# Performance work log

Measured on AMD Instinct MI355X. Metric: run time of the kernel, lower is better.

## Reference

```python
import jax, jax.numpy as jnp
import numpy as np

D_MODEL = 512
D_STATE = 64
N_LAYERS = 6
L_SEQ = 784
BATCH = 64


def _layernorm(x, g, b, eps=1e-5):
    mu = x.mean(-1, keepdims=True)
    var = ((x - mu) ** 2).mean(-1, keepdims=True)
    return (x - mu) * jax.lax.rsqrt(var + eps) * g + b


def _s4d_kernel(log_dt, log_A_real, A_imag, C_re, C_im, L):
    # log_dt: (H,), others: (H, N). Returns real conv kernel (H, L).
    dt = jnp.exp(log_dt)[:, None]                      # (H,1)
    A = -jnp.exp(log_A_real) + 1j * A_imag             # (H,N) complex
    C = C_re + 1j * C_im                               # (H,N)
    dtA = A * dt                                       # (H,N)
    Cd = C * (jnp.exp(dtA) - 1.0) / A                  # ZOH-discretized C
    # Vandermonde: V[h,n,l] = exp(dtA[h,n] * l)
    V = jnp.exp(dtA[:, :, None] * jnp.arange(L, dtype=jnp.float32))  # (H,N,L)
    K = 2.0 * jnp.einsum('hn,hnl->hl', Cd, V).real     # (H,L)
    return K


def _s4_fftconv(u, K, D):
    # u: (B,L,H), K: (H,L), D: (H,)
    L = u.shape[1]
    uf = jnp.fft.rfft(u, 2 * L, axis=1)                # (B, L+1, H)
    kf = jnp.fft.rfft(K.T, 2 * L, axis=0)              # (L+1, H)
    y = jnp.fft.irfft(uf * kf[None], 2 * L, axis=1)[:, :L]
    return y + u * D


def setup_inputs() -> dict:
    key = jax.random.key(0)
    ks = jax.random.split(key, 12)
    H, N, NL = D_MODEL, D_STATE, N_LAYERS
    x = jax.random.normal(ks[0], (BATCH, L_SEQ, 1), dtype=jnp.float32)
    enc_w = jax.random.normal(ks[1], (1, H), dtype=jnp.float32) * 0.5
    enc_b = jnp.zeros((H,), dtype=jnp.float32)
    # S4D-Lin style init, stacked over layers
    log_dt = jnp.tile(
        jax.random.uniform(ks[2], (H,), minval=np.log(0.001), maxval=np.log(0.1)),
        (NL, 1))                                        # (NL,H)
    log_A_real = jnp.full((NL, H, N), jnp.log(0.5), dtype=jnp.float32)
    A_imag = jnp.tile(np.pi * jnp.arange(N, dtype=jnp.float32), (NL, H, 1))
    C_re = jax.random.normal(ks[3], (NL, H, N), dtype=jnp.float32) * (0.5 ** 0.5)
    C_im = jax.random.normal(ks[4], (NL, H, N), dtype=jnp.float32) * (0.5 ** 0.5)
    D = jax.random.normal(ks[5], (NL, H), dtype=jnp.float32)
    ln_g = jnp.ones((NL, H), dtype=jnp.float32)
    ln_b = jnp.zeros((NL, H), dtype=jnp.float32)
    fn_g = jnp.ones((H,), dtype=jnp.float32)
    fn_b = jnp.zeros((H,), dtype=jnp.float32)
    dec_w = jax.random.normal(ks[6], (H, 10), dtype=jnp.float32) / jnp.sqrt(H)
    dec_b = jnp.zeros((10,), dtype=jnp.float32)
    return dict(x=x, enc_w=enc_w, enc_b=enc_b, log_dt=log_dt,
                log_A_real=log_A_real, A_imag=A_imag, C_re=C_re, C_im=C_im,
                D=D, ln_g=ln_g, ln_b=ln_b, fn_g=fn_g, fn_b=fn_b,
                dec_w=dec_w, dec_b=dec_b)


def reference(x, enc_w, enc_b, log_dt, log_A_real, A_imag, C_re, C_im, D,
              ln_g, ln_b, fn_g, fn_b, dec_w, dec_b):
    h = x @ enc_w + enc_b                               # (B,L,H)
    L = h.shape[1]
    for i in range(log_dt.shape[0]):                    # fixed n_layers
        K = _s4d_kernel(log_dt[i], log_A_real[i], A_imag[i], C_re[i], C_im[i], L)
        z = _s4_fftconv(h, K, D[i])                     # S4 output (dropout=eval)
        h = _layernorm(h + z, ln_g[i], ln_b[i])         # residual + LN
    h = _layernorm(h, fn_g, fn_b)
    h = h.mean(axis=1)                                  # mean pool over seq
    return h @ dec_w + dec_b                            # (B,10)
```

## Files before the change

kernel.cpp:

```cpp
#include <hip/hip_runtime.h>
#include <hip/hip_bf16.h>

#define HD 512
#define NST 64
#define NLAY 6
#define LSEQ 784
#define BB 64
#define NKA 848
#define TOFF 800
#define LPADROWS 800
#define KSTR 850
#define CHK2 5
#define NCH 5
#define UTS2 9

typedef unsigned short u16;
typedef short s8v __attribute__((ext_vector_type(8)));
typedef float f16v __attribute__((ext_vector_type(16)));
typedef u16  u4h __attribute__((ext_vector_type(4)));
typedef u16  u8h __attribute__((ext_vector_type(8)));

__device__ __forceinline__ unsigned f2b(float f)
{
    unsigned u = __builtin_bit_cast(unsigned, f);
    return (u + 0x7FFFu + ((u >> 16) & 1u)) >> 16;
}
__device__ __forceinline__ float b2f16(u16 v)
{
    unsigned u = ((unsigned)v) << 16;
    return __builtin_bit_cast(float, u);
}

__global__ void precompute_k(const float* __restrict__ log_dt,
                             const float* __restrict__ log_A_real,
                             const float* __restrict__ A_imag,
                             const float* __restrict__ C_re,
                             const float* __restrict__ C_im,
                             float* __restrict__ lamr, float* __restrict__ lami,
                             float* __restrict__ dtr,  float* __restrict__ dti,
                             float* __restrict__ c2r,  float* __restrict__ c2i)
{
    int t = blockIdx.x * 256 + threadIdx.x;
    if (t >= NLAY * HD * NST) return;
    int ih = t >> 6;
    float dt  = expf(log_dt[ih]);
    float are = -expf(log_A_real[t]);
    float aim = A_imag[t];
    float dr = are * dt, di = aim * dt;
    float er = expf(dr);
    float sn, cs; __sincosf(di, &sn, &cs);
    float lr = er * cs, li = er * sn;
    float e1r = lr - 1.0f, e1i = li;
    float den = are * are + aim * aim;
    float qr = (e1r * are + e1i * aim) / den;
    float qi = (e1i * are - e1r * aim) / den;
    float crv = C_re[t], civ = C_im[t];
    lamr[t] = lr; lami[t] = li; dtr[t] = dr; dti[t] = di;
    c2r[t] = 2.0f * (crv * qr - civ * qi);
    c2i[t] = 2.0f * (crv * qi + civ * qr);
}

__global__ void kq_k(const float* __restrict__ lamr, const float* __restrict__ lami,
                     const float* __restrict__ dtr,  const float* __restrict__ dti,
                     const float* __restrict__ c2r,  const float* __restrict__ c2i,
                     u16* __restrict__ KA)
{
    int t = blockIdx.x * 256 + threadIdx.x;
    int dc = t % 49;
    int ih = t / 49;
    int d0 = dc * 16;
    float acc[16];
#pragma unroll
    for (int k = 0; k < 16; k++) acc[k] = 0.f;
    int base = ih * 64;
    for (int n = 0; n < 64; n += 4) {
        float lr[4], li[4], cr[4], ci[4], pr[4], pi[4];
#pragma unroll
        for (int j = 0; j < 4; j++) {
            int q = base + n + j;
            lr[j] = lamr[q]; li[j] = lami[q];
            float dr = dtr[q], di = dti[q];
            cr[j] = c2r[q]; ci[j] = c2i[q];
            float e = __expf(dr * (float)d0);
            float sn, cs; __sincosf(di * (float)d0, &sn, &cs);
            pr[j] = e * cs; pi[j] = e * sn;
        }
#pragma unroll
        for (int k = 0; k < 16; k++) {
#pragma unroll
            for (int j = 0; j < 4; j++) {
                acc[k] = fmaf(cr[j], pr[j], fmaf(-ci[j], pi[j], acc[k]));
                float nr = pr[j] * lr[j] - pi[j] * li[j];
                pi[j] = fmaf(pr[j], li[j], pi[j] * lr[j]);
                pr[j] = nr;
            }
        }
    }
    u16* kap = KA + (size_t)ih * NKA;
#pragma unroll
    for (int k = 0; k < 16; k++)
        kap[TOFF - (d0 + k)] = (u16)f2b(acc[k]);
    if (dc == 0)  for (int z = TOFF + 1; z < NKA; z++) kap[z] = 0;
    if (dc == 48) for (int z = 0; z < TOFF - 783; z++) kap[z] = 0;
}

__global__ void xt_k(const float* __restrict__ x, float* __restrict__ xT)
{
    int t = blockIdx.x * 256 + threadIdx.x;
    int l = t >> 6, b = t & 63;
    xT[t] = x[b * LSEQ + l];
}

__global__ void encoder_k(const float* __restrict__ xT, const float* __restrict__ ew,
                          const float* __restrict__ eb, u16* __restrict__ Vb)
{
    int g = blockIdx.x * 256 + threadIdx.x;
    int bo = g & 7;
    int h  = (g >> 3) & 511;
    int l  = g >> 12;
    uint4* dst = (uint4*)&Vb[((size_t)l * HD + h) * BB + 8 * bo];
    if (l >= LSEQ) { *dst = (uint4){0, 0, 0, 0}; return; }
    const float4* xp = (const float4*)&xT[l * BB + 8 * bo];
    float4 a0 = xp[0], a1 = xp[1];
    float w = ew[h], bb = eb[h];
    unsigned p0 = f2b(fmaf(a0.x, w, bb)) | (f2b(fmaf(a0.y, w, bb)) << 16);
    unsigned p1 = f2b(fmaf(a0.z, w, bb)) | (f2b(fmaf(a0.w, w, bb)) << 16);
    unsigned p2 = f2b(fmaf(a1.x, w, bb)) | (f2b(fmaf(a1.y, w, bb)) << 16);
    unsigned p3 = f2b(fmaf(a1.z, w, bb)) | (f2b(fmaf(a1.w, w, bb)) << 16);
    *dst = (uint4){p0, p1, p2, p3};
}

__global__ __launch_bounds__(128, 4)
void conv_k(const u16* __restrict__ Vb, u16* __restrict__ V2,
            const u16* __restrict__ KA, const float* __restrict__ Dvec)
{
    __shared__ __align__(16) u16 KR[6816];
    __shared__ __align__(16) unsigned UT[2][64 * UTS2];

    const int thr = threadIdx.x;
    const int h   = blockIdx.x & 511;
    const int c   = NCH - 1 - (blockIdx.x >> 9);
    const int w   = thr >> 6;
    const int lane = thr & 63;
    const int n2 = lane & 31;
    const int qp = lane >> 5;
    const int JTN = 10 * c + 10;

    const u16* kap = KA + (size_t)h * NKA;
    {
        int s = thr & 7, ch = thr >> 3;
        int i0 = ch * 53;
        int i1 = (i0 + 53 < NKA) ? (i0 + 53) : NKA;
        u16* kr = KR + KSTR * s + ((8 - s) & 7);
        for (int i = i0; i < i1; i++) kr[i] = kap[i];
    }

    const int jj = thr >> 4;
    const int bq = thr & 15;
    {
        const u16* p = &Vb[((size_t)(2 * jj) * HD + h) * BB + 4 * bq];
        u4h r0 = *(const u4h*)p;
        u4h r1 = *(const u4h*)(p + (size_t)HD * BB);
        unsigned* up = &UT[0][0];
#pragma unroll
        for (int i = 0; i < 4; i++)
            up[(4 * bq + i) * UTS2 + jj] = (unsigned)r0[i] | ((unsigned)r1[i] << 16);
    }
    __syncthreads();

    f16v acc[CHK2];
#pragma unroll
    for (int i = 0; i < CHK2; i++)
#pragma unroll
        for (int r = 0; r < 16; r++) acc[i][r] = 0.f;

    const float dcoef = 1.0f + Dvec[h];

    const int s = lane & 7;
    const u16* krb = KR + KSTR * s + ((8 - s) & 7)
                     + (TOFF - 160 * c) + 8 * qp - n2;
    const unsigned* bb0 = &UT[0][(32 * w + n2) * UTS2 + 4 * qp];
    const unsigned* bb1 = &UT[1][(32 * w + n2) * UTS2 + 4 * qp];

    for (int jt = 0; jt < JTN; ++jt) {
        u4h r0, r1;
        const bool more = (jt + 1) < JTN;
        if (more) {
            int j = 16 * (jt + 1) + 2 * jj;
            const u16* p = &Vb[((size_t)j * HD + h) * BB + 4 * bq];
            r0 = *(const u4h*)p;
            r1 = *(const u4h*)(p + (size_t)HD * BB);
        }
        const unsigned* bb = (jt & 1) ? bb1 : bb0;
        union { unsigned u[4]; s8v v; } bu;
        bu.u[0] = bb[0]; bu.u[1] = bb[1]; bu.u[2] = bb[2]; bu.u[3] = bb[3];

        const u16* ap0 = krb + 16 * jt;
#pragma unroll
        for (int lt = 0; lt < CHK2; ++lt) {
            if (jt > 10 * c + 2 * lt + 1) continue;
            s8v av = *(const s8v*)__builtin_assume_aligned(ap0 - 32 * lt, 16);
            acc[lt] = __builtin_amdgcn_mfma_f32_32x32x16_bf16(av, bu.v, acc[lt], 0, 0, 0);
        }
        if (more) {
            unsigned* up = &UT[(jt & 1) ^ 1][0];
#pragma unroll
            for (int i = 0; i < 4; i++)
                up[(4 * bq + i) * UTS2 + jj] = (unsigned)r0[i] | ((unsigned)r1[i] << 16);
        }
        __syncthreads();
    }

#pragma unroll
    for (int lt = 0; lt < CHK2; ++lt) {
        const int l0 = 32 * (5 * c + lt) + 4 * qp;
#pragma unroll
        for (int r = 0; r < 16; ++r) {
            int l = l0 + (r & 3) + 8 * (r >> 2);
            size_t a = ((size_t)l * HD + h) * BB + 32 * w + n2;
            V2[a] = (u16)f2b(fmaf(dcoef, b2f16(Vb[a]), acc[lt][r]));
        }
    }
}

__global__ __launch_bounds__(512)
void lnT_k(const u16* __restrict__ src, u16* __restrict__ dst,
           const float* __restrict__ gp, const float* __restrict__ bp)
{
    __shared__ float redS[64][65], redQ[64][65];
    __shared__ float mus[64], rss[64];
    __shared__ float gs[512], bs[512];
    const int thr = threadIdx.x;
    const int bo = thr & 7;
    const int hg = thr >> 3;
    const size_t l = blockIdx.x;
    gs[thr] = gp[thr]; bs[thr] = bp[thr];

    const u16* sp = &src[(l * HD + hg * 8) * BB + 8 * bo];
    float v[64];
    float s[8] = {0, 0, 0, 0, 0, 0, 0, 0};
    float q[8] = {0, 0, 0, 0, 0, 0, 0, 0};
#pragma unroll
    for (int k = 0; k < 8; k++) {
        u8h r = *(const u8h*)(sp + (size_t)k * BB);
#pragma unroll
        for (int i = 0; i < 8; i++) {
            float x = b2f16(r[i]);
            v[k * 8 + i] = x;
            s[i] += x;
            q[i] = fmaf(x, x, q[i]);
        }
    }
#pragma unroll
    for (int i = 0; i < 8; i++) { redS[hg][8 * bo + i] = s[i]; redQ[hg][8 * bo + i] = q[i]; }
    __syncthreads();
    if (thr < 64) {
        float ts = 0.f, tq = 0.f;
#pragma unroll
        for (int g = 0; g < 64; g++) { ts += redS[g][thr]; tq += redQ[g][thr]; }
        float mu = ts * (1.0f / HD);
        mus[thr] = mu;
        rss[thr] = rsqrtf(tq * (1.0f / HD) - mu * mu + 1e-5f);
    }
    __syncthreads();
    float mu[8], rs[8];
#pragma unroll
    for (int i = 0; i < 8; i++) { mu[i] = mus[8 * bo + i]; rs[i] = rss[8 * bo + i]; }
    u16* dp = &dst[(l * HD + hg * 8) * BB + 8 * bo];
#pragma unroll
    for (int k = 0; k < 8; k++) {
        float g = gs[hg * 8 + k], bb = bs[hg * 8 + k];
        u8h w;
#pragma unroll
        for (int i = 0; i < 8; i++)
            w[i] = (u16)f2b(fmaf((v[k * 8 + i] - mu[i]) * rs[i], g, bb));
        *(u8h*)(dp + (size_t)k * BB) = w;
    }
}

__global__ __launch_bounds__(512)
void lnT2s_k(const u16* __restrict__ src, u16* __restrict__ dst,
             const float* __restrict__ g5p, const float* __restrict__ b5p,
             const float* __restrict__ gp, const float* __restrict__ bp)
{
    __shared__ float redS[64][65], redQ[64][65];
    __shared__ float mu1s[64], rs1s[64], mu2s[64], rs2s[64];
    __shared__ float gs[512], bs[512];
    const int thr = threadIdx.x;
    const int bo = thr & 7;
    const int hg = thr >> 3;
    const size_t l = blockIdx.x;
    gs[thr] = gp[thr]; bs[thr] = bp[thr];

    const u16* sp = &src[(l * HD + (size_t)hg * 8) * BB + 8 * bo];
    float v[64];
    float s[8] = {0, 0, 0, 0, 0, 0, 0, 0};
    float q[8] = {0, 0, 0, 0, 0, 0, 0, 0};
#pragma unroll
    for (int k = 0; k < 8; k++) {
        u8h r = *(const u8h*)(sp + (size_t)k * BB);
#pragma unroll
        for (int i = 0; i < 8; i++) {
            float x = b2f16(r[i]);
            v[k * 8 + i] = x;
            s[i] += x;
            q[i] = fmaf(x, x, q[i]);
        }
    }
#pragma unroll
    for (int i = 0; i < 8; i++) { redS[hg][8 * bo + i] = s[i]; redQ[hg][8 * bo + i] = q[i]; }
    __syncthreads();
    if (thr < 64) {
        float ts = 0.f, tq = 0.f;
#pragma unroll
        for (int g = 0; g < 64; g++) { ts += redS[g][thr]; tq += redQ[g][thr]; }
        float mu = ts * (1.0f / HD);
        mu1s[thr] = mu;
        rs1s[thr] = rsqrtf(tq * (1.0f / HD) - mu * mu + 1e-5f);
    }
    __syncthreads();
    float mu1[8], rs1[8];
#pragma unroll
    for (int i = 0; i < 8; i++) { mu1[i] = mu1s[8 * bo + i]; rs1[i] = rs1s[8 * bo + i]; }

    float s2[8] = {0, 0, 0, 0, 0, 0, 0, 0};
    float q2[8] = {0, 0, 0, 0, 0, 0, 0, 0};
#pragma unroll
    for (int k = 0; k < 8; k++) {
        float g5 = g5p[hg * 8 + k], b5 = b5p[hg * 8 + k];
#pragma unroll
        for (int i = 0; i < 8; i++) {
            float x = fmaf((v[k * 8 + i] - mu1[i]) * rs1[i], g5, b5);
            v[k * 8 + i] = x;
            s2[i] += x;
            q2[i] = fmaf(x, x, q2[i]);
        }
    }
#pragma unroll
    for (int i = 0; i < 8; i++) { redS[hg][8 * bo + i] = s2[i]; redQ[hg][8 * bo + i] = q2[i]; }
    __syncthreads();
    if (thr < 64) {
        float ts = 0.f, tq = 0.f;
#pragma unroll
        for (int g = 0; g < 64; g++) { ts += redS[g][thr]; tq += redQ[g][thr]; }
        float mu = ts * (1.0f / HD);
        mu2s[thr] = mu;
        rs2s[thr] = rsqrtf(tq * (1.0f / HD) - mu * mu + 1e-5f);
    }
    __syncthreads();
    float mu2[8], rs2[8];
#pragma unroll
    for (int i = 0; i < 8; i++) { mu2[i] = mu2s[8 * bo + i]; rs2[i] = rs2s[8 * bo + i]; }
    u16* dp = &dst[(l * HD + (size_t)hg * 8) * BB + 8 * bo];
#pragma unroll
    for (int k = 0; k < 8; k++) {
        float g = gs[hg * 8 + k], bb = bs[hg * 8 + k];
        u8h wv;
#pragma unroll
        for (int i = 0; i < 8; i++)
            wv[i] = (u16)f2b(fmaf((v[k * 8 + i] - mu2[i]) * rs2[i], g, bb));
        *(u8h*)(dp + (size_t)k * BB) = wv;
    }
}

__global__ __launch_bounds__(256)
void pool2_k(const u16* __restrict__ Vb, float* __restrict__ PO2)
{
    const int cb = blockIdx.x & 15;
    const int lg = blockIdx.x >> 4;
    const int off = cb * 2048 + threadIdx.x * 8;
    const u16* p = Vb + (size_t)(lg * 49) * (HD * BB) + off;
    float s[8] = {0, 0, 0, 0, 0, 0, 0, 0};
    for (int l = 0; l < 49; l++) {
        u8h r = *(const u8h*)p;
        p += HD * BB;
#pragma unroll
        for (int i = 0; i < 8; i++) s[i] += b2f16(r[i]);
    }
    float* q = PO2 + (size_t)lg * (HD * BB) + off;
    *(float4*)q       = (float4){s[0], s[1], s[2], s[3]};
    *(float4*)(q + 4) = (float4){s[4], s[5], s[6], s[7]};
}

__global__ void poolr_k(const float* __restrict__ PO2, float* __restrict__ PO)
{
    int t = blockIdx.x * 256 + threadIdx.x;
    float s = 0.f;
#pragma unroll
    for (int g = 0; g < 16; g++) s += PO2[(size_t)g * (HD * BB) + t];
    PO[t] = s * (1.0f / LSEQ);
}

__global__ void dec_k(const float* __restrict__ PO, const float* __restrict__ w,
                      const float* __restrict__ bias, float* __restrict__ out)
{
    int t = blockIdx.x * 256 + threadIdx.x;
    if (t >= BB * 10) return;
    int cc = t % 10, b = t / 10;
    float acc = bias[cc];
    for (int hh = 0; hh < HD; hh++)
        acc = fmaf(PO[hh * BB + b], w[hh * 10 + cc], acc);
    out[t] = acc;
}

extern "C" void kernel_launch(void* const* d_in, const int* in_sizes, int n_in,
                              void* d_out, int out_size, void* d_ws, size_t ws_size,
                              hipStream_t stream)
{
    const float* x   = (const float*)d_in[0];
    const float* ew  = (const float*)d_in[1];
    const float* eb  = (const float*)d_in[2];
    const float* ldt = (const float*)d_in[3];
    const float* lar = (const float*)d_in[4];
    const float* aim = (const float*)d_in[5];
    const float* cre = (const float*)d_in[6];
    const float* cim = (const float*)d_in[7];
    const float* Dp  = (const float*)d_in[8];
    const float* lng = (const float*)d_in[9];
    const float* lnb = (const float*)d_in[10];
    const float* fng = (const float*)d_in[11];
    const float* fnb = (const float*)d_in[12];
    const float* dw  = (const float*)d_in[13];
    const float* db  = (const float*)d_in[14];
    float* out = (float*)d_out;

    const size_t SZB = (size_t)BB * LPADROWS * HD;
    const size_t PP  = (size_t)NLAY * HD * NST;
    u16*   Vb  = (u16*)d_ws;
    u16*   V2  = Vb + SZB;
    float* PAR = (float*)(V2 + SZB);
    float* lamr = PAR,        * lami = PAR + PP;
    float* dtr  = PAR + 2*PP, * dti  = PAR + 3*PP;
    float* c2r  = PAR + 4*PP, * c2i  = PAR + 5*PP;
    u16* KA = (u16*)(PAR + 6 * PP);
    float* PO = PAR + 6 * PP + (NLAY * HD * NKA) / 2;
    float* xT = PO + BB * HD;
    float* PO2 = xT + LSEQ * BB;

    precompute_k<<<(NLAY * HD * NST + 255) / 256, 256, 0, stream>>>(
        ldt, lar, aim, cre, cim, lamr, lami, dtr, dti, c2r, c2i);
    kq_k<<<(NLAY * HD * 49) / 256, 256, 0, stream>>>(
        lamr, lami, dtr, dti, c2r, c2i, KA);
    xt_k<<<(LSEQ * BB) / 256, 256, 0, stream>>>(x, xT);
    encoder_k<<<(LPADROWS * HD * 8) / 256, 256, 0, stream>>>(xT, ew, eb, Vb);

    for (int i = 0; i < NLAY - 1; i++) {
        conv_k<<<512 * NCH, 128, 0, stream>>>(
            Vb, V2, KA + (size_t)i * HD * NKA, Dp + i * HD);
        lnT_k<<<LSEQ, 512, 0, stream>>>(V2, Vb, lng + i * HD, lnb + i * HD);
    }
    conv_k<<<512 * NCH, 128, 0, stream>>>(
        Vb, V2, KA + (size_t)5 * HD * NKA, Dp + 5 * HD);
    lnT2s_k<<<LSEQ, 512, 0, stream>>>(V2, Vb, lng + 5 * HD, lnb + 5 * HD, fng, fnb);

    pool2_k<<<256, 256, 0, stream>>>(Vb, PO2);
    poolr_k<<<(HD * BB) / 256, 256, 0, stream>>>(PO2, PO);
    dec_k<<<(BB * 10 + 255) / 256, 256, 0, stream>>>(PO, dw, db, out);
}
```

Measured before the change: 554.0 us.

## Use wave shuffles for LayerNorm reductions and hardware bf16 pack conversion

The LayerNorm kernels now reduce per-batch sums across the hidden groups inside each wave with xor shuffles. Only 8 partial rows per block go to shared memory instead of 64, which cuts LDS traffic and shortens the serial 64-step final reduction to 8 steps. The bf16 rounding in the encoder and LN outputs now uses the v_cvt_pk_bf16_f32 instruction instead of manual integer rounding. The kq kernel unrolls 8 states per iteration instead of 4, which raises register use. The extra barrier added before reusing shared memory in the second LN pass keeps the result correct.

```diff
diff --git a/kernel.cpp b/kernel.cpp
--- a/kernel.cpp
+++ b/kernel.cpp
@@ -29,6 +29,12 @@
 {
     unsigned u = ((unsigned)v) << 16;
     return __builtin_bit_cast(float, u);
+}
+__device__ __forceinline__ unsigned pkbf(float lo, float hi)
+{
+    unsigned r;
+    asm("v_cvt_pk_bf16_f32 %0, %1, %2" : "=v"(r) : "v"(lo), "v"(hi));
+    return r;
 }
 
 __global__ void precompute_k(const float* __restrict__ log_dt,
@@ -73,10 +79,10 @@
 #pragma unroll
     for (int k = 0; k < 16; k++) acc[k] = 0.f;
     int base = ih * 64;
-    for (int n = 0; n < 64; n += 4) {
-        float lr[4], li[4], cr[4], ci[4], pr[4], pi[4];
-#pragma unroll
-        for (int j = 0; j < 4; j++) {
+    for (int n = 0; n < 64; n += 8) {
+        float lr[8], li[8], cr[8], ci[8], pr[8], pi[8];
+#pragma unroll
+        for (int j = 0; j < 8; j++) {
             int q = base + n + j;
             lr[j] = lamr[q]; li[j] = lami[q];
             float dr = dtr[q], di = dti[q];
@@ -88,7 +94,7 @@
 #pragma unroll
         for (int k = 0; k < 16; k++) {
 #pragma unroll
-            for (int j = 0; j < 4; j++) {
+            for (int j = 0; j < 8; j++) {
                 acc[k] = fmaf(cr[j], pr[j], fmaf(-ci[j], pi[j], acc[k]));
                 float nr = pr[j] * lr[j] - pi[j] * li[j];
                 pi[j] = fmaf(pr[j], li[j], pi[j] * lr[j]);
@@ -123,10 +129,10 @@
     const float4* xp = (const float4*)&xT[l * BB + 8 * bo];
     float4 a0 = xp[0], a1 = xp[1];
     float w = ew[h], bb = eb[h];
-    unsigned p0 = f2b(fmaf(a0.x, w, bb)) | (f2b(fmaf(a0.y, w, bb)) << 16);
-    unsigned p1 = f2b(fmaf(a0.z, w, bb)) | (f2b(fmaf(a0.w, w, bb)) << 16);
-    unsigned p2 = f2b(fmaf(a1.x, w, bb)) | (f2b(fmaf(a1.y, w, bb)) << 16);
-    unsigned p3 = f2b(fmaf(a1.z, w, bb)) | (f2b(fmaf(a1.w, w, bb)) << 16);
+    unsigned p0 = pkbf(fmaf(a0.x, w, bb), fmaf(a0.y, w, bb));
+    unsigned p1 = pkbf(fmaf(a0.z, w, bb), fmaf(a0.w, w, bb));
+    unsigned p2 = pkbf(fmaf(a1.x, w, bb), fmaf(a1.y, w, bb));
+    unsigned p3 = pkbf(fmaf(a1.z, w, bb), fmaf(a1.w, w, bb));
     *dst = (uint4){p0, p1, p2, p3};
 }
 
@@ -227,10 +233,12 @@
 void lnT_k(const u16* __restrict__ src, u16* __restrict__ dst,
            const float* __restrict__ gp, const float* __restrict__ bp)
 {
-    __shared__ float redS[64][65], redQ[64][65];
+    __shared__ float redS[8][64], redQ[8][64];
     __shared__ float mus[64], rss[64];
     __shared__ float gs[512], bs[512];
     const int thr = threadIdx.x;
+    const int lane = thr & 63;
+    const int wv = thr >> 6;
     const int bo = thr & 7;
     const int hg = thr >> 3;
     const size_t l = blockIdx.x;
@@ -252,12 +260,23 @@
         }
     }
 #pragma unroll
-    for (int i = 0; i < 8; i++) { redS[hg][8 * bo + i] = s[i]; redQ[hg][8 * bo + i] = q[i]; }
+    for (int i = 0; i < 8; i++) {
+        s[i] += __shfl_xor(s[i], 8);  q[i] += __shfl_xor(q[i], 8);
+        s[i] += __shfl_xor(s[i], 16); q[i] += __shfl_xor(q[i], 16);
+        s[i] += __shfl_xor(s[i], 32); q[i] += __shfl_xor(q[i], 32);
+    }
+    if (lane < 8) {
+#pragma unroll
+        for (int i = 0; i < 8; i++) {
+            redS[wv][8 * lane + i] = s[i];
+            redQ[wv][8 * lane + i] = q[i];
+        }
+    }
     __syncthreads();
     if (thr < 64) {
         float ts = 0.f, tq = 0.f;
 #pragma unroll
-        for (int g = 0; g < 64; g++) { ts += redS[g][thr]; tq += redQ[g][thr]; }
+        for (int g = 0; g < 8; g++) { ts += redS[g][thr]; tq += redQ[g][thr]; }
         float mu = ts * (1.0f / HD);
         mus[thr] = mu;
         rss[thr] = rsqrtf(tq * (1.0f / HD) - mu * mu + 1e-5f);
@@ -270,11 +289,13 @@
 #pragma unroll
     for (int k = 0; k < 8; k++) {
         float g = gs[hg * 8 + k], bb = bs[hg * 8 + k];
-        u8h w;
+        float y[8];
 #pragma unroll
         for (int i = 0; i < 8; i++)
-            w[i] = (u16)f2b(fmaf((v[k * 8 + i] - mu[i]) * rs[i], g, bb));
-        *(u8h*)(dp + (size_t)k * BB) = w;
+            y[i] = fmaf((v[k * 8 + i] - mu[i]) * rs[i], g, bb);
+        uint4 pkt = {pkbf(y[0], y[1]), pkbf(y[2], y[3]),
+                     pkbf(y[4], y[5]), pkbf(y[6], y[7])};
+        *(uint4*)(dp + (size_t)k * BB) = pkt;
     }
 }
 
@@ -283,10 +304,12 @@
              const float* __restrict__ g5p, const float* __restrict__ b5p,
              const float* __restrict__ gp, const float* __restrict__ bp)
 {
-    __shared__ float redS[64][65], redQ[64][65];
+    __shared__ float redS[8][64], redQ[8][64];
     __shared__ float mu1s[64], rs1s[64], mu2s[64], rs2s[64];
     __shared__ float gs[512], bs[512];
     const int thr = threadIdx.x;
+    const int lane = thr & 63;
+    const int wv = thr >> 6;
     const int bo = thr & 7;
     const int hg = thr >> 3;
     const size_t l = blockIdx.x;
@@ -308,12 +331,23 @@
         }
     }
 #pragma unroll
-    for (int i = 0; i < 8; i++) { redS[hg][8 * bo + i] = s[i]; redQ[hg][8 * bo + i] = q[i]; }
+    for (int i = 0; i < 8; i++) {
+        s[i] += __shfl_xor(s[i], 8);  q[i] += __shfl_xor(q[i], 8);
+        s[i] += __shfl_xor(s[i], 16); q[i] += __shfl_xor(q[i], 16);
+        s[i] += __shfl_xor(s[i], 32); q[i] += __shfl_xor(q[i], 32);
+    }
+    if (lane < 8) {
+#pragma unroll
+        for (int i = 0; i < 8; i++) {
+            redS[wv][8 * lane + i] = s[i];
+            redQ[wv][8 * lane + i] = q[i];
+        }
+    }
     __syncthreads();
     if (thr < 64) {
         float ts = 0.f, tq = 0.f;
 #pragma unroll
-        for (int g = 0; g < 64; g++) { ts += redS[g][thr]; tq += redQ[g][thr]; }
+        for (int g = 0; g < 8; g++) { ts += redS[g][thr]; tq += redQ[g][thr]; }
         float mu = ts * (1.0f / HD);
         mu1s[thr] = mu;
         rs1s[thr] = rsqrtf(tq * (1.0f / HD) - mu * mu + 1e-5f);
@@ -337,12 +371,24 @@
         }
     }
 #pragma unroll
-    for (int i = 0; i < 8; i++) { redS[hg][8 * bo + i] = s2[i]; redQ[hg][8 * bo + i] = q2[i]; }
+    for (int i = 0; i < 8; i++) {
+        s2[i] += __shfl_xor(s2[i], 8);  q2[i] += __shfl_xor(q2[i], 8);
+        s2[i] += __shfl_xor(s2[i], 16); q2[i] += __shfl_xor(q2[i], 16);
+        s2[i] += __shfl_xor(s2[i], 32); q2[i] += __shfl_xor(q2[i], 32);
+    }
+    __syncthreads();
+    if (lane < 8) {
+#pragma unroll
+        for (int i = 0; i < 8; i++) {
+            redS[wv][8 * lane + i] = s2[i];
+            redQ[wv][8 * lane + i] = q2[i];
+        }
+    }
     __syncthreads();
     if (thr < 64) {
         float ts = 0.f, tq = 0.f;
 #pragma unroll
-        for (int g = 0; g < 64; g++) { ts += redS[g][thr]; tq += redQ[g][thr]; }
+        for (int g = 0; g < 8; g++) { ts += redS[g][thr]; tq += redQ[g][thr]; }
         float mu = ts * (1.0f / HD);
         mu2s[thr] = mu;
         rs2s[thr] = rsqrtf(tq * (1.0f / HD) - mu * mu + 1e-5f);
@@ -355,11 +401,13 @@
 #pragma unroll
     for (int k = 0; k < 8; k++) {
         float g = gs[hg * 8 + k], bb = bs[hg * 8 + k];
-        u8h wv;
+        float y[8];
 #pragma unroll
         for (int i = 0; i < 8; i++)
-            wv[i] = (u16)f2b(fmaf((v[k * 8 + i] - mu2[i]) * rs2[i], g, bb));
-        *(u8h*)(dp + (size_t)k * BB) = wv;
+            y[i] = fmaf((v[k * 8 + i] - mu2[i]) * rs2[i], g, bb);
+        uint4 pkt = {pkbf(y[0], y[1]), pkbf(y[2], y[3]),
+                     pkbf(y[4], y[5]), pkbf(y[6], y[7])};
+        *(uint4*)(dp + (size_t)k * BB) = pkt;
     }
 }
 
```

After: 623.1 us. 1.12x slower.
